# Kernel optimization log

Measured on AMD Instinct MI355X. Metric: run time of the kernel, lower is better.

Reference implementation:

```python
import jax, jax.numpy as jnp
import numpy as np

BS, DIM = 131072, 256

def setup_inputs() -> dict:
    key = jax.random.key(0)
    ks = jax.random.split(key, 5)
    scale = 1.0 / np.sqrt(DIM)
    return {
        "z": jax.random.normal(ks[0], (BS, DIM), dtype=jnp.float32),
        "W_mu": jax.random.normal(ks[1], (DIM, DIM), dtype=jnp.float32) * scale,
        "b_mu": jax.random.normal(ks[2], (DIM,), dtype=jnp.float32) * scale,
        "W_std": jax.random.normal(ks[3], (DIM, DIM), dtype=jnp.float32) * scale,
        "b_std": jax.random.normal(ks[4], (DIM,), dtype=jnp.float32) * scale,
    }

def reference(z, W_mu, b_mu, W_std, b_std):
    # Linear + ReLU projections (torch Linear: y = x @ W.T + b)
    mu = jax.nn.relu(z @ W_mu.T + b_mu)            # [bs, dim]
    log_std = jax.nn.relu(z @ W_std.T + b_std)     # [bs, dim], std = exp(log_std)
    # Closed-form KL(p || q), p = N(0, I), q = N(mu, diag(std^2)):
    # 0.5 * sum( 1/var + mu^2/var - 1 + log var ), var = exp(2*log_std)
    inv_var = jnp.exp(-2.0 * log_std)
    kl_per_sample = 0.5 * jnp.sum((1.0 + mu * mu) * inv_var - 1.0 + 2.0 * log_std, axis=-1)
    kl = jnp.mean(kl_per_sample)                   # scalar, batch-averaged
    z_out = mu[:, None, :]                         # mode(mu, std).unsqueeze(1)
    return z_out, kl
```

## Files before the change

kernel.cpp:

```cpp
#include <hip/hip_runtime.h>
#include <hip/hip_bf16.h>

#define BSZ  131072
#define DIM  256
#define ROWS 32
#define NT   1024
#define NBLK 256
#define TPB  (BSZ / ROWS / NBLK)

typedef __attribute__((ext_vector_type(8))) short bf16x8;
typedef __attribute__((ext_vector_type(4))) float f32x4;
typedef __attribute__((ext_vector_type(4))) unsigned int u32x4;
typedef __attribute__((ext_vector_type(4))) unsigned short u16x4;

#define ZSTR  528
#define OSTR  1040
#define OBASE 33792

__device__ __forceinline__ unsigned short f2bf(float f) {
  unsigned u = __builtin_bit_cast(unsigned, f);
  return (unsigned short)((u + 0x7FFFu + ((u >> 16) & 1u)) >> 16);
}
__device__ __forceinline__ unsigned cvt_pk(float lo, float hi) {
  unsigned r;
  asm("v_cvt_pk_bf16_f32 %0, %1, %2" : "=v"(r) : "v"(lo), "v"(hi));
  return r;
}

__global__ void prep_kernel(const float* __restrict__ Wmu, const float* __restrict__ Wsd,
                            unsigned short* __restrict__ wm, unsigned short* __restrict__ wsd) {
  const int tg = blockIdx.x * 256 + threadIdx.x;
  const int j  = tg >> 6, kq = tg & 63;
  const int dst = ((kq >> 3) << 13) + (j << 5) + ((kq & 7) << 2);
  f32x4 a = *(const f32x4*)(Wmu + j * 256 + kq * 4);
  f32x4 b = *(const f32x4*)(Wsd + j * 256 + kq * 4);
  u16x4 pa, pb;
#pragma unroll
  for (int e = 0; e < 4; ++e) { pa[e] = f2bf(a[e]); pb[e] = f2bf(b[e]); }
  *(u16x4*)(wm + dst)  = pa;
  *(u16x4*)(wsd + dst) = pb;
}

__global__ __launch_bounds__(NT, 4)
void main_kernel(const float* __restrict__ z,
                 const unsigned short* __restrict__ wm,
                 const unsigned short* __restrict__ wsd,
                 const float* __restrict__ bmu,
                 const float* __restrict__ bsd,
                 float* __restrict__ out,
                 float* __restrict__ partials) {
  __shared__ unsigned char smem[67072];
  __shared__ float redbuf[16];
  const int t = threadIdx.x, lane = t & 63, w = t >> 6;
  const int bid = blockIdx.x;

  const int woff = (w * 16 + (lane & 15)) * 32 + (lane >> 4) * 8;
  bf16x8 wfm[8], wfs[8];
#pragma unroll
  for (int kb = 0; kb < 8; ++kb) {
    wfm[kb] = *(const bf16x8*)(wm  + (kb << 13) + woff);
    wfs[kb] = *(const bf16x8*)(wsd + (kb << 13) + woff);
  }
  const int colb = w * 16 + ((lane >> 4) << 2);
  const f32x4 b4m = *(const f32x4*)(bmu + colb);
  const f32x4 b4s = *(const f32x4*)(bsd + colb);

  const int zrow = t >> 5, zc = t & 31;
  const int zwofs = zrow * ZSTR + zc * 16;
  const int zro   = (lane & 15) * ZSTR + (lane >> 4) * 16;
  const int ow    = (lane & 15) * OSTR + colb * 4;

  const size_t TSTEP = (size_t)NBLK * ROWS * DIM;
  const float* zp = z + (size_t)(bid * ROWS + zrow) * DIM + zc * 8;
  float* op = out + (size_t)(bid * ROWS) * DIM;

  float klp = 0.0f;
  f32x4 pza, pzb;

  {
    f32x4 a = *(const f32x4*)zp;
    f32x4 b = *(const f32x4*)(zp + 4);
    u32x4 p;
    p[0] = cvt_pk(a[0], a[1]); p[1] = cvt_pk(a[2], a[3]);
    p[2] = cvt_pk(b[0], b[1]); p[3] = cvt_pk(b[2], b[3]);
    *(u32x4*)(smem + zwofs) = p;
  }
  pza = *(const f32x4*)(zp + TSTEP);
  pzb = *(const f32x4*)(zp + TSTEP + 4);
  asm volatile("s_waitcnt lgkmcnt(0)" ::: "memory");
  __builtin_amdgcn_sched_barrier(0);
  __builtin_amdgcn_s_barrier();

#pragma unroll 1
  for (int i = 0; i < TPB; ++i) {
    const unsigned char* zb = smem + ((i & 1) ? 16896 : 0);

    f32x4 am[2], al[2];
    am[0] = (f32x4)0.0f; am[1] = (f32x4)0.0f;
    al[0] = (f32x4)0.0f; al[1] = (f32x4)0.0f;

#pragma unroll
    for (int kb = 0; kb < 8; ++kb)
#pragma unroll
      for (int nj = 0; nj < 2; ++nj) {
        const bf16x8 zf = *(const bf16x8*)(zb + nj * 16 * ZSTR + kb * 64 + zro);
        am[nj] = __builtin_amdgcn_mfma_f32_16x16x32_bf16(wfm[kb], zf, am[nj], 0, 0, 0);
        al[nj] = __builtin_amdgcn_mfma_f32_16x16x32_bf16(wfs[kb], zf, al[nj], 0, 0, 0);
      }

#pragma unroll
    for (int nj = 0; nj < 2; ++nj) {
      f32x4 mu4;
#pragma unroll
      for (int r = 0; r < 4; ++r) {
        float mu = fmaxf(am[nj][r] + b4m[r], 0.0f);
        float ls = fmaxf(al[nj][r] + b4s[r], 0.0f);
        float iv = __expf(-2.0f * ls);
        klp += fmaf(mu * mu, iv, iv) + 2.0f * ls;
        mu4[r] = mu;
      }
      *(f32x4*)(smem + OBASE + nj * 16 * OSTR + ow) = mu4;
    }
    asm volatile("s_waitcnt lgkmcnt(0)" ::: "memory");
    __builtin_amdgcn_sched_barrier(0);
    __builtin_amdgcn_s_barrier();

#pragma unroll
    for (int rr = 0; rr < 2; ++rr) {
      const int row = w * 2 + rr;
      const f32x4 v = *(const f32x4*)(smem + OBASE + row * OSTR + lane * 16);
      __builtin_nontemporal_store(v, (f32x4*)(op + (size_t)i * TSTEP + row * DIM + lane * 4));
    }

    if (i < TPB - 1) {
      u32x4 p;
      p[0] = cvt_pk(pza[0], pza[1]); p[1] = cvt_pk(pza[2], pza[3]);
      p[2] = cvt_pk(pzb[0], pzb[1]); p[3] = cvt_pk(pzb[2], pzb[3]);
      *(u32x4*)(smem + (((i + 1) & 1) ? 16896 : 0) + zwofs) = p;
    }
    if (i < TPB - 2) {
      pza = *(const f32x4*)(zp + (size_t)(i + 2) * TSTEP);
      pzb = *(const f32x4*)(zp + (size_t)(i + 2) * TSTEP + 4);
    }
    asm volatile("s_waitcnt lgkmcnt(0)" ::: "memory");
    __builtin_amdgcn_sched_barrier(0);
    __builtin_amdgcn_s_barrier();
  }

  klp = 0.5f * (klp - (float)(TPB * 8));
#pragma unroll
  for (int off = 32; off; off >>= 1) klp += __shfl_down(klp, off);
  if (lane == 0) redbuf[w] = klp;
  __syncthreads();
  if (t == 0) {
    float s = 0.0f;
#pragma unroll
    for (int i = 0; i < 16; ++i) s += redbuf[i];
    partials[bid] = s;
  }
}

__global__ void fin_kernel(const float* __restrict__ partials, float* __restrict__ out) {
  __shared__ double red[256];
  double s = (double)partials[threadIdx.x];
  red[threadIdx.x] = s;
  __syncthreads();
  for (int st = 128; st > 0; st >>= 1) {
    if ((int)threadIdx.x < st) red[threadIdx.x] += red[threadIdx.x + st];
    __syncthreads();
  }
  if (threadIdx.x == 0) out[(size_t)BSZ * DIM] = (float)(red[0] / (double)BSZ);
}

extern "C" void kernel_launch(void* const* d_in, const int* in_sizes, int n_in,
                              void* d_out, int out_size, void* d_ws, size_t ws_size,
                              hipStream_t stream) {
  const float* z   = (const float*)d_in[0];
  const float* Wmu = (const float*)d_in[1];
  const float* bmu = (const float*)d_in[2];
  const float* Wsd = (const float*)d_in[3];
  const float* bsd = (const float*)d_in[4];
  float* out = (float*)d_out;

  float* partials     = (float*)d_ws;
  unsigned short* wm  = (unsigned short*)((char*)d_ws + 16384);
  unsigned short* wsd = wm + DIM * DIM;

  prep_kernel<<<64, 256, 0, stream>>>(Wmu, Wsd, wm, wsd);
  main_kernel<<<NBLK, NT, 0, stream>>>(z, wm, wsd, bmu, bsd, out, partials);
  fin_kernel<<<1, 256, 0, stream>>>(partials, out);
}
```

Baseline: 59.21 us.

## Double rows per block tile and restructure z prefetch to one-step lookahead

Each block iteration now processes 64 rows instead of 32, so every wave issues four MFMA column tiles per weight fragment and there are half as many loop iterations and barriers. The z staging buffers and output buffer double in LDS, to about 134 KB, and each thread loads 16 floats per step. The prefetch distance drops from two steps ahead to one, with the loads for the next step issued at the top of the loop. This aims to amortise barrier and per-iteration overhead across more MFMA work, at the cost of more LDS, more registers and less latency hiding on the global z loads.

```diff
diff --git a/kernel.cpp b/kernel.cpp
--- a/kernel.cpp
+++ b/kernel.cpp
@@ -3,7 +3,7 @@
 
 #define BSZ  131072
 #define DIM  256
-#define ROWS 32
+#define ROWS 64
 #define NT   1024
 #define NBLK 256
 #define TPB  (BSZ / ROWS / NBLK)
@@ -15,7 +15,8 @@
 
 #define ZSTR  528
 #define OSTR  1040
-#define OBASE 33792
+#define ZB(b) ((b) * 33792)
+#define OBASE 67584
 
 __device__ __forceinline__ unsigned short f2bf(float f) {
   unsigned u = __builtin_bit_cast(unsigned, f);
@@ -49,7 +50,7 @@
                  const float* __restrict__ bsd,
                  float* __restrict__ out,
                  float* __restrict__ partials) {
-  __shared__ unsigned char smem[67072];
+  __shared__ unsigned char smem[134144];
   __shared__ float redbuf[16];
   const int t = threadIdx.x, lane = t & 63, w = t >> 6;
   const int bid = blockIdx.x;
@@ -65,51 +66,56 @@
   const f32x4 b4m = *(const f32x4*)(bmu + colb);
   const f32x4 b4s = *(const f32x4*)(bsd + colb);
 
-  const int zrow = t >> 5, zc = t & 31;
-  const int zwofs = zrow * ZSTR + zc * 16;
+  const int zrow = t >> 4, zc16 = t & 15;
+  const int zwofs = zrow * ZSTR + zc16 * 32;
   const int zro   = (lane & 15) * ZSTR + (lane >> 4) * 16;
   const int ow    = (lane & 15) * OSTR + colb * 4;
 
   const size_t TSTEP = (size_t)NBLK * ROWS * DIM;
-  const float* zp = z + (size_t)(bid * ROWS + zrow) * DIM + zc * 8;
+  const float* zp = z + (size_t)(bid * ROWS + zrow) * DIM + zc16 * 16;
   float* op = out + (size_t)(bid * ROWS) * DIM;
 
   float klp = 0.0f;
-  f32x4 pza, pzb;
+  f32x4 zc[4];
 
+#pragma unroll
+  for (int j = 0; j < 4; ++j) zc[j] = *(const f32x4*)(zp + j * 4);
   {
-    f32x4 a = *(const f32x4*)zp;
-    f32x4 b = *(const f32x4*)(zp + 4);
-    u32x4 p;
-    p[0] = cvt_pk(a[0], a[1]); p[1] = cvt_pk(a[2], a[3]);
-    p[2] = cvt_pk(b[0], b[1]); p[3] = cvt_pk(b[2], b[3]);
-    *(u32x4*)(smem + zwofs) = p;
+    u32x4 p0, p1;
+    p0[0] = cvt_pk(zc[0][0], zc[0][1]); p0[1] = cvt_pk(zc[0][2], zc[0][3]);
+    p0[2] = cvt_pk(zc[1][0], zc[1][1]); p0[3] = cvt_pk(zc[1][2], zc[1][3]);
+    p1[0] = cvt_pk(zc[2][0], zc[2][1]); p1[1] = cvt_pk(zc[2][2], zc[2][3]);
+    p1[2] = cvt_pk(zc[3][0], zc[3][1]); p1[3] = cvt_pk(zc[3][2], zc[3][3]);
+    *(u32x4*)(smem + ZB(0) + zwofs) = p0;
+    *(u32x4*)(smem + ZB(0) + zwofs + 16) = p1;
   }
-  pza = *(const f32x4*)(zp + TSTEP);
-  pzb = *(const f32x4*)(zp + TSTEP + 4);
   asm volatile("s_waitcnt lgkmcnt(0)" ::: "memory");
   __builtin_amdgcn_sched_barrier(0);
   __builtin_amdgcn_s_barrier();
 
 #pragma unroll 1
   for (int i = 0; i < TPB; ++i) {
-    const unsigned char* zb = smem + ((i & 1) ? 16896 : 0);
+    if (i < TPB - 1) {
+#pragma unroll
+      for (int j = 0; j < 4; ++j)
+        zc[j] = *(const f32x4*)(zp + (size_t)(i + 1) * TSTEP + j * 4);
+    }
 
-    f32x4 am[2], al[2];
-    am[0] = (f32x4)0.0f; am[1] = (f32x4)0.0f;
-    al[0] = (f32x4)0.0f; al[1] = (f32x4)0.0f;
-
+    const unsigned char* zb = smem + ZB(i & 1);
+    f32x4 am[4], al[4];
+#pragma unroll
+    for (int nj = 0; nj < 4; ++nj) { am[nj] = (f32x4)0.0f; al[nj] = (f32x4)0.0f; }
 #pragma unroll
     for (int kb = 0; kb < 8; ++kb)
 #pragma unroll
-      for (int nj = 0; nj < 2; ++nj) {
+      for (int nj = 0; nj < 4; ++nj) {
         const bf16x8 zf = *(const bf16x8*)(zb + nj * 16 * ZSTR + kb * 64 + zro);
         am[nj] = __builtin_amdgcn_mfma_f32_16x16x32_bf16(wfm[kb], zf, am[nj], 0, 0, 0);
         al[nj] = __builtin_amdgcn_mfma_f32_16x16x32_bf16(wfs[kb], zf, al[nj], 0, 0, 0);
       }
 
 #pragma unroll
-    for (int nj = 0; nj < 2; ++nj) {
+    for (int nj = 0; nj < 4; ++nj) {
       f32x4 mu4;
 #pragma unroll
       for (int r = 0; r < 4; ++r) {
@@ -121,33 +127,34 @@
       }
       *(f32x4*)(smem + OBASE + nj * 16 * OSTR + ow) = mu4;
     }
+
     asm volatile("s_waitcnt lgkmcnt(0)" ::: "memory");
     __builtin_amdgcn_sched_barrier(0);
     __builtin_amdgcn_s_barrier();
 
 #pragma unroll
-    for (int rr = 0; rr < 2; ++rr) {
-      const int row = w * 2 + rr;
+    for (int rr = 0; rr < 4; ++rr) {
+      const int row = w * 4 + rr;
       const f32x4 v = *(const f32x4*)(smem + OBASE + row * OSTR + lane * 16);
       __builtin_nontemporal_store(v, (f32x4*)(op + (size_t)i * TSTEP + row * DIM + lane * 4));
     }
 
     if (i < TPB - 1) {
-      u32x4 p;
-      p[0] = cvt_pk(pza[0], pza[1]); p[1] = cvt_pk(pza[2], pza[3]);
-      p[2] = cvt_pk(pzb[0], pzb[1]); p[3] = cvt_pk(pzb[2], pzb[3]);
-      *(u32x4*)(smem + (((i + 1) & 1) ? 16896 : 0) + zwofs) = p;
+      u32x4 p0, p1;
+      p0[0] = cvt_pk(zc[0][0], zc[0][1]); p0[1] = cvt_pk(zc[0][2], zc[0][3]);
+      p0[2] = cvt_pk(zc[1][0], zc[1][1]); p0[3] = cvt_pk(zc[1][2], zc[1][3]);
+      p1[0] = cvt_pk(zc[2][0], zc[2][1]); p1[1] = cvt_pk(zc[2][2], zc[2][3]);
+      p1[2] = cvt_pk(zc[3][0], zc[3][1]); p1[3] = cvt_pk(zc[3][2], zc[3][3]);
+      *(u32x4*)(smem + ZB((i + 1) & 1) + zwofs) = p0;
+      *(u32x4*)(smem + ZB((i + 1) & 1) + zwofs + 16) = p1;
     }
-    if (i < TPB - 2) {
-      pza = *(const f32x4*)(zp + (size_t)(i + 2) * TSTEP);
-      pzb = *(const f32x4*)(zp + (size_t)(i + 2) * TSTEP + 4);
-    }
+
     asm volatile("s_waitcnt lgkmcnt(0)" ::: "memory");
     __builtin_amdgcn_sched_barrier(0);
     __builtin_amdgcn_s_barrier();
   }
 
-  klp = 0.5f * (klp - (float)(TPB * 8));
+  klp = 0.5f * (klp - (float)(TPB * 16));
 #pragma unroll
   for (int off = 32; off; off >>= 1) klp += __shfl_down(klp, off);
   if (lane == 0) redbuf[w] = klp;
@@ -162,8 +169,7 @@
 
 __global__ void fin_kernel(const float* __restrict__ partials, float* __restrict__ out) {
   __shared__ double red[256];
-  double s = (double)partials[threadIdx.x];
-  red[threadIdx.x] = s;
+  red[threadIdx.x] = (double)partials[threadIdx.x];
   __syncthreads();
   for (int st = 128; st > 0; st >>= 1) {
     if ((int)threadIdx.x < st) red[threadIdx.x] += red[threadIdx.x + st];
```

Measured after the change: 116.9 us. 97.4% more time.

## Split output columns across block pairs with swizzled unpadded z tiles in LDS

Applied to the files above, without the earlier changes.

Each block now covers half of the 256 output columns with 512 threads, and twice as many blocks run, so each pair of blocks shares a row group. The z tile in LDS drops its padding and uses an XOR swizzle to avoid bank conflicts. The prefetch of the next z tile now happens at the start of each iteration with 16-float loads per thread. The cost is that every z row is loaded and converted twice, once per column half, and the final reduction now sums 512 partials. An unused staging lambda is left in the code.

```diff
diff --git a/kernel.cpp b/kernel.cpp
--- a/kernel.cpp
+++ b/kernel.cpp
@@ -4,18 +4,19 @@
 #define BSZ  131072
 #define DIM  256
 #define ROWS 32
-#define NT   1024
-#define NBLK 256
-#define TPB  (BSZ / ROWS / NBLK)
+#define NT   512
+#define NBLK 512
+#define TPB  16
 
 typedef __attribute__((ext_vector_type(8))) short bf16x8;
 typedef __attribute__((ext_vector_type(4))) float f32x4;
 typedef __attribute__((ext_vector_type(4))) unsigned int u32x4;
 typedef __attribute__((ext_vector_type(4))) unsigned short u16x4;
 
-#define ZSTR  528
-#define OSTR  1040
-#define OBASE 33792
+#define ZSTRD 512
+#define OSTR  528
+#define ZB(b) ((b) * 16384)
+#define OBASE 32768
 
 __device__ __forceinline__ unsigned short f2bf(float f) {
   unsigned u = __builtin_bit_cast(unsigned, f);
@@ -49,64 +50,88 @@
                  const float* __restrict__ bsd,
                  float* __restrict__ out,
                  float* __restrict__ partials) {
-  __shared__ unsigned char smem[67072];
-  __shared__ float redbuf[16];
+  __shared__ unsigned char smem[49664];
+  __shared__ float redbuf[8];
   const int t = threadIdx.x, lane = t & 63, w = t >> 6;
   const int bid = blockIdx.x;
-
-  const int woff = (w * 16 + (lane & 15)) * 32 + (lane >> 4) * 8;
+  const int ch  = bid & 1;
+  const int rg0 = bid >> 1;
+
+  const int gcol0 = ch * 128 + w * 16;
+  const int woff = (gcol0 + (lane & 15)) * 32 + (lane >> 4) * 8;
   bf16x8 wfm[8], wfs[8];
 #pragma unroll
   for (int kb = 0; kb < 8; ++kb) {
     wfm[kb] = *(const bf16x8*)(wm  + (kb << 13) + woff);
     wfs[kb] = *(const bf16x8*)(wsd + (kb << 13) + woff);
   }
-  const int colb = w * 16 + ((lane >> 4) << 2);
-  const f32x4 b4m = *(const f32x4*)(bmu + colb);
-  const f32x4 b4s = *(const f32x4*)(bsd + colb);
-
-  const int zrow = t >> 5, zc = t & 31;
-  const int zwofs = zrow * ZSTR + zc * 16;
-  const int zro   = (lane & 15) * ZSTR + (lane >> 4) * 16;
-  const int ow    = (lane & 15) * OSTR + colb * 4;
-
-  const size_t TSTEP = (size_t)NBLK * ROWS * DIM;
-  const float* zp = z + (size_t)(bid * ROWS + zrow) * DIM + zc * 8;
-  float* op = out + (size_t)(bid * ROWS) * DIM;
+  const int gcolb = gcol0 + ((lane >> 4) << 2);
+  const int lcolb = w * 16 + ((lane >> 4) << 2);
+  const f32x4 b4m = *(const f32x4*)(bmu + gcolb);
+  const f32x4 b4s = *(const f32x4*)(bsd + gcolb);
+
+  const int zrow = t >> 4, zc16 = t & 15;
+  const size_t TSTEP = (size_t)256 * ROWS * DIM;
+  const float* zp = z + (size_t)(rg0 * ROWS + zrow) * DIM + zc16 * 16;
+  float* op = out + (size_t)(rg0 * ROWS) * DIM;
+
+  const int zrbase = (lane & 15) * ZSTRD;
+  const int g = lane >> 4, r7 = lane & 7;
+
+  const int ow = (lane & 15) * OSTR + lcolb * 4;
 
   float klp = 0.0f;
-  f32x4 pza, pzb;
-
-  {
-    f32x4 a = *(const f32x4*)zp;
-    f32x4 b = *(const f32x4*)(zp + 4);
+  f32x4 zc[4];
+
+  auto stage = [&](int i, int buf) {
+#pragma unroll
+    for (int j = 0; j < 4; ++j) {
+      u32x4 p;
+      p[0] = cvt_pk(zc[j][0], zc[j][1]); p[1] = cvt_pk(zc[j][2], zc[j][3]);
+      const int slot = (zc16 * 4 + j) ^ (zrow & 7);
+      *(unsigned long long*)(smem + ZB(buf) + zrow * ZSTRD + slot * 16) =
+          *(unsigned long long*)&p;
+      (void)p;
+    }
+  };
+  (void)stage;
+
+#pragma unroll
+  for (int j = 0; j < 4; ++j) zc[j] = *(const f32x4*)(zp + j * 4);
+#pragma unroll
+  for (int j = 0; j < 2; ++j) {
     u32x4 p;
-    p[0] = cvt_pk(a[0], a[1]); p[1] = cvt_pk(a[2], a[3]);
-    p[2] = cvt_pk(b[0], b[1]); p[3] = cvt_pk(b[2], b[3]);
-    *(u32x4*)(smem + zwofs) = p;
-  }
-  pza = *(const f32x4*)(zp + TSTEP);
-  pzb = *(const f32x4*)(zp + TSTEP + 4);
+    p[0] = cvt_pk(zc[2*j][0], zc[2*j][1]);   p[1] = cvt_pk(zc[2*j][2], zc[2*j][3]);
+    p[2] = cvt_pk(zc[2*j+1][0], zc[2*j+1][1]); p[3] = cvt_pk(zc[2*j+1][2], zc[2*j+1][3]);
+    const int slot = (zc16 * 2 + j) ^ (zrow & 7);
+    *(u32x4*)(smem + ZB(0) + zrow * ZSTRD + slot * 16) = p;
+  }
   asm volatile("s_waitcnt lgkmcnt(0)" ::: "memory");
   __builtin_amdgcn_sched_barrier(0);
   __builtin_amdgcn_s_barrier();
 
 #pragma unroll 1
   for (int i = 0; i < TPB; ++i) {
-    const unsigned char* zb = smem + ((i & 1) ? 16896 : 0);
-
+    if (i < TPB - 1) {
+#pragma unroll
+      for (int j = 0; j < 4; ++j)
+        zc[j] = *(const f32x4*)(zp + (size_t)(i + 1) * TSTEP + j * 4);
+    }
+
+    const unsigned char* zb = smem + ZB(i & 1);
     f32x4 am[2], al[2];
     am[0] = (f32x4)0.0f; am[1] = (f32x4)0.0f;
     al[0] = (f32x4)0.0f; al[1] = (f32x4)0.0f;
-
-#pragma unroll
-    for (int kb = 0; kb < 8; ++kb)
+#pragma unroll
+    for (int kb = 0; kb < 8; ++kb) {
+      const int slot = ((kb << 2) | g) ^ r7;
 #pragma unroll
       for (int nj = 0; nj < 2; ++nj) {
-        const bf16x8 zf = *(const bf16x8*)(zb + nj * 16 * ZSTR + kb * 64 + zro);
+        const bf16x8 zf = *(const bf16x8*)(zb + nj * 16 * ZSTRD + zrbase + slot * 16);
         am[nj] = __builtin_amdgcn_mfma_f32_16x16x32_bf16(wfm[kb], zf, am[nj], 0, 0, 0);
         al[nj] = __builtin_amdgcn_mfma_f32_16x16x32_bf16(wfs[kb], zf, al[nj], 0, 0, 0);
       }
+    }
 
 #pragma unroll
     for (int nj = 0; nj < 2; ++nj) {
@@ -121,27 +146,30 @@
       }
       *(f32x4*)(smem + OBASE + nj * 16 * OSTR + ow) = mu4;
     }
+
     asm volatile("s_waitcnt lgkmcnt(0)" ::: "memory");
     __builtin_amdgcn_sched_barrier(0);
     __builtin_amdgcn_s_barrier();
 
 #pragma unroll
     for (int rr = 0; rr < 2; ++rr) {
-      const int row = w * 2 + rr;
-      const f32x4 v = *(const f32x4*)(smem + OBASE + row * OSTR + lane * 16);
-      __builtin_nontemporal_store(v, (f32x4*)(op + (size_t)i * TSTEP + row * DIM + lane * 4));
+      const int row = w * 4 + rr * 2 + (lane >> 5);
+      const f32x4 v = *(const f32x4*)(smem + OBASE + row * OSTR + (lane & 31) * 16);
+      __builtin_nontemporal_store(v,
+          (f32x4*)(op + (size_t)i * TSTEP + row * DIM + ch * 128 + (lane & 31) * 4));
     }
 
     if (i < TPB - 1) {
-      u32x4 p;
-      p[0] = cvt_pk(pza[0], pza[1]); p[1] = cvt_pk(pza[2], pza[3]);
-      p[2] = cvt_pk(pzb[0], pzb[1]); p[3] = cvt_pk(pzb[2], pzb[3]);
-      *(u32x4*)(smem + (((i + 1) & 1) ? 16896 : 0) + zwofs) = p;
-    }
-    if (i < TPB - 2) {
-      pza = *(const f32x4*)(zp + (size_t)(i + 2) * TSTEP);
-      pzb = *(const f32x4*)(zp + (size_t)(i + 2) * TSTEP + 4);
-    }
+#pragma unroll
+      for (int j = 0; j < 2; ++j) {
+        u32x4 p;
+        p[0] = cvt_pk(zc[2*j][0], zc[2*j][1]);     p[1] = cvt_pk(zc[2*j][2], zc[2*j][3]);
+        p[2] = cvt_pk(zc[2*j+1][0], zc[2*j+1][1]); p[3] = cvt_pk(zc[2*j+1][2], zc[2*j+1][3]);
+        const int slot = (zc16 * 2 + j) ^ (zrow & 7);
+        *(u32x4*)(smem + ZB((i + 1) & 1) + zrow * ZSTRD + slot * 16) = p;
+      }
+    }
+
     asm volatile("s_waitcnt lgkmcnt(0)" ::: "memory");
     __builtin_amdgcn_sched_barrier(0);
     __builtin_amdgcn_s_barrier();
@@ -155,15 +183,14 @@
   if (t == 0) {
     float s = 0.0f;
 #pragma unroll
-    for (int i = 0; i < 16; ++i) s += redbuf[i];
+    for (int i = 0; i < 8; ++i) s += redbuf[i];
     partials[bid] = s;
   }
 }
 
 __global__ void fin_kernel(const float* __restrict__ partials, float* __restrict__ out) {
   __shared__ double red[256];
-  double s = (double)partials[threadIdx.x];
-  red[threadIdx.x] = s;
+  red[threadIdx.x] = (double)partials[threadIdx.x] + (double)partials[threadIdx.x + 256];
   __syncthreads();
   for (int st = 128; st > 0; st >>= 1) {
     if ((int)threadIdx.x < st) red[threadIdx.x] += red[threadIdx.x + st];
```

Result: slower. 79.25 us (+33.8%).
